# Performance work log

Hardware: AMD Instinct MI355X
Metric: run time of the kernel (lower is better)

## Reference

```python
import jax, jax.numpy as jnp
import numpy as np

B, D, K = 16384, 256, 1024

def setup_inputs() -> dict:
    key = jax.random.key(0)
    k1, k2 = jax.random.split(key)
    x = jax.random.normal(k1, (B, D), dtype=jnp.float32)
    centers = jax.random.uniform(k2, (K, D), dtype=jnp.float32)  # RandomUniform(0,1)
    betas = jnp.ones((K,), dtype=jnp.float32)
    return {"x": x, "centers": centers, "betas": betas}

def reference(x, centers, betas):
    x_sq = jnp.sum(x * x, axis=-1, keepdims=True)          # [B,1]
    c_sq = jnp.sum(centers * centers, axis=-1)             # [K]
    cross = jnp.einsum('bd,kd->bk', x, centers)            # [B,K]
    diffnorm = x_sq + c_sq[None, :] - 2.0 * cross          # [B,K]
    return jnp.exp(-betas[None, :] * diffnorm)             # [B,K]
```

## Files before the change

kernel.cpp:

```cpp
#include <hip/hip_runtime.h>
#include <stdint.h>

#define D_DIM 256
#define K_CTR 1024
#define B_ROWS 16384
#define BM 32

typedef float f32x4 __attribute__((ext_vector_type(4)));
typedef float f32x2 __attribute__((ext_vector_type(2)));
typedef long long i64x2 __attribute__((ext_vector_type(2)));

static __device__ __forceinline__ unsigned cvt4_fp8(const float4 v) {
    int r = __builtin_amdgcn_cvt_pk_fp8_f32(v.x, v.y, 0, false);
    r = __builtin_amdgcn_cvt_pk_fp8_f32(v.z, v.w, r, true);
    return (unsigned)r;
}

static __device__ __forceinline__ void barrier_lgkm() {
    asm volatile("s_waitcnt lgkmcnt(0)" ::: "memory");
    __builtin_amdgcn_s_barrier();
}

__global__ __launch_bounds__(256) void rbf_prep(const float* __restrict__ centers,
                                                unsigned char* __restrict__ cbf,
                                                float* __restrict__ csq) {
    const int w = threadIdx.x >> 6;
    const int l = threadIdx.x & 63;
    const int c0 = blockIdx.x * 4 + w;
    const float4 v = *reinterpret_cast<const float4*>(centers + c0 * D_DIM + l * 4);
    float s = v.x * v.x + v.y * v.y + v.z * v.z + v.w * v.w;
    const unsigned u = cvt4_fp8(v);
    const unsigned off = (unsigned)((c0 >> 4) * 4096 + (l >> 4) * 1024
                       + (((l >> 1) & 3) * 16 + (c0 & 15)) * 16
                       + ((l >> 3) & 1) * 8 + (l & 1) * 4);
    *reinterpret_cast<unsigned*>(cbf + off) = u;
    #pragma unroll
    for (int off2 = 1; off2 < 64; off2 <<= 1) s += __shfl_xor(s, off2);
    if (l == 0) csq[c0] = s;
}

__global__ __launch_bounds__(512, 4) void rbf_main(const float* __restrict__ x,
                                                   const unsigned char* __restrict__ cbf,
                                                   const float* __restrict__ csq,
                                                   const float* __restrict__ betas,
                                                   float* __restrict__ out) {
    __shared__ __align__(16) unsigned char As[BM * D_DIM];
    __shared__ __align__(16) float obuf[2][BM * 128];
    __shared__ float xs_lds[BM];

    const int tid = threadIdx.x;
    const int w = tid >> 6;
    const int l = tid & 63;
    const int strip = (blockIdx.x & 7) * 64 + (blockIdx.x >> 3);
    const int row0 = strip * BM;

    #pragma unroll
    for (int i = 0; i < 4; ++i) {
        const int r = i * 8 + w;
        const float4 v = *reinterpret_cast<const float4*>(x + (size_t)(row0 + r) * D_DIM + l * 4);
        float s = v.x * v.x + v.y * v.y + v.z * v.z + v.w * v.w;
        const unsigned u = cvt4_fp8(v);
        const unsigned pos = (unsigned)((l >> 4) * 64 + ((l >> 1) & 3) * 16
                           + ((l >> 3) & 1) * 8 + (l & 1) * 4);
        *reinterpret_cast<unsigned*>(As + r * 256 + (pos ^ ((unsigned)(r & 7) << 4))) = u;
        #pragma unroll
        for (int off = 1; off < 64; off <<= 1) s += __shfl_xor(s, off);
        if (l == 0) xs_lds[r] = s;
    }

    const int hk = l >> 4;
    const int lr = l & 15;
    const unsigned char* bwave = cbf + l * 16;

    i64x2 b0[4], b1[4];
    {
        const unsigned char* bbase = bwave + w * 4096;
        #pragma unroll
        for (int p = 0; p < 4; ++p)
            b0[p] = *reinterpret_cast<const i64x2*>(bbase + p * 1024);
    }
    barrier_lgkm();

    i64x2 a[2][4];
    #pragma unroll
    for (int m = 0; m < 2; ++m) {
        const int r = m * 16 + lr;
        #pragma unroll
        for (int p = 0; p < 4; ++p)
            a[m][p] = *reinterpret_cast<const i64x2*>(
                As + r * 256 + ((unsigned)(p * 64 + hk * 16) ^ ((unsigned)(lr & 7) << 4)));
    }
    const float xs0 = xs_lds[lr];
    const float xs1 = xs_lds[16 + lr];
    const float LOG2E = 1.4426950408889634f;

    #pragma unroll
    for (int ph = 0; ph < 8; ++ph) {
        const int colp = ph * 128;
        const i64x2 (&bc)[4] = (ph & 1) ? b1 : b0;
        i64x2 (&bn)[4] = (ph & 1) ? b0 : b1;

        if (ph < 7) {
            const unsigned char* bbase = bwave + ((ph + 1) * 8 + w) * 4096;
            #pragma unroll
            for (int p = 0; p < 4; ++p)
                bn[p] = *reinterpret_cast<const i64x2*>(bbase + p * 1024);
        }

        f32x4 acc[2] = {};
        #pragma unroll
        for (int p = 0; p < 4; ++p)
            #pragma unroll
            for (int m = 0; m < 2; ++m) {
                acc[m] = __builtin_amdgcn_mfma_f32_16x16x32_fp8_fp8(bc[p][0], a[m][p][0], acc[m], 0, 0, 0);
                acc[m] = __builtin_amdgcn_mfma_f32_16x16x32_fp8_fp8(bc[p][1], a[m][p][1], acc[m], 0, 0, 0);
            }

        float* ob = obuf[ph & 1];
        {
            const int cl = w * 16 + hk * 4;
            const f32x4 cs = *reinterpret_cast<const f32x4*>(csq + colp + cl);
            const f32x4 bt = *reinterpret_cast<const f32x4*>(betas + colp + cl);
            f32x4 btl2, coef2, base;
            #pragma unroll
            for (int j = 0; j < 4; ++j) {
                btl2[j] = bt[j] * LOG2E;
                coef2[j] = btl2[j] + btl2[j];
                base[j] = -btl2[j] * cs[j];
            }
            #pragma unroll
            for (int m = 0; m < 2; ++m) {
                const int r = m * 16 + lr;
                const float xsv = m ? xs1 : xs0;
                f32x4 rv;
                #pragma unroll
                for (int j = 0; j < 4; ++j) {
                    const float c0 = __builtin_fmaf(-btl2[j], xsv, base[j]);
                    rv[j] = __builtin_exp2f(__builtin_fmaf(coef2[j], acc[m][j], c0));
                }
                *reinterpret_cast<f32x4*>(reinterpret_cast<char*>(ob)
                    + r * 512 + ((unsigned)(cl * 4) ^ ((unsigned)(r & 7) << 4))) = rv;
            }
        }
        barrier_lgkm();

        #pragma unroll
        for (int i = 0; i < 4; ++i) {
            const int r = w * 4 + i;
            const f32x2 v = *reinterpret_cast<const f32x2*>(reinterpret_cast<const char*>(obuf[ph & 1])
                    + r * 512 + ((unsigned)(l * 8) ^ ((unsigned)(r & 7) << 4)));
            *reinterpret_cast<f32x2*>(out + (size_t)(row0 + r) * K_CTR + colp + l * 2) = v;
        }
    }
}

extern "C" void kernel_launch(void* const* d_in, const int* in_sizes, int n_in,
                              void* d_out, int out_size, void* d_ws, size_t ws_size,
                              hipStream_t stream) {
    const float* x       = (const float*)d_in[0];
    const float* centers = (const float*)d_in[1];
    const float* betas   = (const float*)d_in[2];
    float* out = (float*)d_out;

    unsigned char* cbf = (unsigned char*)d_ws;
    float* csq = (float*)((char*)d_ws + (size_t)K_CTR * D_DIM);

    rbf_prep<<<K_CTR / 4, 256, 0, stream>>>(centers, cbf, csq);
    rbf_main<<<B_ROWS / BM, 512, 0, stream>>>(x, cbf, csq, betas, out);
}
```

Measured before the change: 27.33 us.

## Restructure output staging into two full-row passes with 16-byte global stores

The main loop is reorganised so each 16-row half of the tile computes all 1024 columns before writing. Results are staged in a larger 64KB LDS buffer and flushed as whole rows with 128-bit global stores, replacing the per-128-column 64-bit stores. This cuts the barrier count from 8 to about 3 and makes the write stream more contiguous. The cost is doubled B-fragment reloads from global/L2 (16 phases instead of 8), half the MFMA work between loads, and more LDS per block, which may lower occupancy below the launch-bounds target.

```diff
diff --git a/kernel.cpp b/kernel.cpp
--- a/kernel.cpp
+++ b/kernel.cpp
@@ -7,7 +7,6 @@
 #define BM 32
 
 typedef float f32x4 __attribute__((ext_vector_type(4)));
-typedef float f32x2 __attribute__((ext_vector_type(2)));
 typedef long long i64x2 __attribute__((ext_vector_type(2)));
 
 static __device__ __forceinline__ unsigned cvt4_fp8(const float4 v) {
@@ -45,7 +44,7 @@
                                                    const float* __restrict__ betas,
                                                    float* __restrict__ out) {
     __shared__ __align__(16) unsigned char As[BM * D_DIM];
-    __shared__ __align__(16) float obuf[2][BM * 128];
+    __shared__ __align__(16) float obuf[16 * K_CTR];
     __shared__ float xs_lds[BM];
 
     const int tid = threadIdx.x;
@@ -83,74 +82,68 @@
 
     i64x2 a[2][4];
     #pragma unroll
-    for (int m = 0; m < 2; ++m) {
-        const int r = m * 16 + lr;
+    for (int s = 0; s < 2; ++s) {
+        const int r = s * 16 + lr;
         #pragma unroll
         for (int p = 0; p < 4; ++p)
-            a[m][p] = *reinterpret_cast<const i64x2*>(
+            a[s][p] = *reinterpret_cast<const i64x2*>(
                 As + r * 256 + ((unsigned)(p * 64 + hk * 16) ^ ((unsigned)(lr & 7) << 4)));
     }
-    const float xs0 = xs_lds[lr];
-    const float xs1 = xs_lds[16 + lr];
+    const float xsA[2] = { xs_lds[lr], xs_lds[16 + lr] };
     const float LOG2E = 1.4426950408889634f;
 
     #pragma unroll
-    for (int ph = 0; ph < 8; ++ph) {
-        const int colp = ph * 128;
-        const i64x2 (&bc)[4] = (ph & 1) ? b1 : b0;
-        i64x2 (&bn)[4] = (ph & 1) ? b0 : b1;
+    for (int s = 0; s < 2; ++s) {
+        #pragma unroll
+        for (int ph = 0; ph < 8; ++ph) {
+            const int t = s * 8 + ph;
+            const i64x2 (&bc)[4] = (t & 1) ? b1 : b0;
+            i64x2 (&bn)[4] = (t & 1) ? b0 : b1;
 
-        if (ph < 7) {
-            const unsigned char* bbase = bwave + ((ph + 1) * 8 + w) * 4096;
-            #pragma unroll
-            for (int p = 0; p < 4; ++p)
-                bn[p] = *reinterpret_cast<const i64x2*>(bbase + p * 1024);
-        }
-
-        f32x4 acc[2] = {};
-        #pragma unroll
-        for (int p = 0; p < 4; ++p)
-            #pragma unroll
-            for (int m = 0; m < 2; ++m) {
-                acc[m] = __builtin_amdgcn_mfma_f32_16x16x32_fp8_fp8(bc[p][0], a[m][p][0], acc[m], 0, 0, 0);
-                acc[m] = __builtin_amdgcn_mfma_f32_16x16x32_fp8_fp8(bc[p][1], a[m][p][1], acc[m], 0, 0, 0);
+            if (t < 15) {
+                const unsigned char* bbase = bwave + (((t + 1) & 7) * 8 + w) * 4096;
+                #pragma unroll
+                for (int p = 0; p < 4; ++p)
+                    bn[p] = *reinterpret_cast<const i64x2*>(bbase + p * 1024);
             }
 
-        float* ob = obuf[ph & 1];
-        {
-            const int cl = w * 16 + hk * 4;
-            const f32x4 cs = *reinterpret_cast<const f32x4*>(csq + colp + cl);
-            const f32x4 bt = *reinterpret_cast<const f32x4*>(betas + colp + cl);
-            f32x4 btl2, coef2, base;
+            f32x4 acc = {};
+            #pragma unroll
+            for (int p = 0; p < 4; ++p) {
+                acc = __builtin_amdgcn_mfma_f32_16x16x32_fp8_fp8(bc[p][0], a[s][p][0], acc, 0, 0, 0);
+                acc = __builtin_amdgcn_mfma_f32_16x16x32_fp8_fp8(bc[p][1], a[s][p][1], acc, 0, 0, 0);
+            }
+
+            const int cl = ph * 128 + w * 16 + hk * 4;
+            const f32x4 cs = *reinterpret_cast<const f32x4*>(csq + cl);
+            const f32x4 bt = *reinterpret_cast<const f32x4*>(betas + cl);
+            f32x4 rv;
             #pragma unroll
             for (int j = 0; j < 4; ++j) {
-                btl2[j] = bt[j] * LOG2E;
-                coef2[j] = btl2[j] + btl2[j];
-                base[j] = -btl2[j] * cs[j];
+                const float btl2 = bt[j] * LOG2E;
+                const float c0 = -btl2 * (xsA[s] + cs[j]);
+                rv[j] = __builtin_exp2f(__builtin_fmaf(btl2 + btl2, acc[j], c0));
             }
-            #pragma unroll
-            for (int m = 0; m < 2; ++m) {
-                const int r = m * 16 + lr;
-                const float xsv = m ? xs1 : xs0;
-                f32x4 rv;
-                #pragma unroll
-                for (int j = 0; j < 4; ++j) {
-                    const float c0 = __builtin_fmaf(-btl2[j], xsv, base[j]);
-                    rv[j] = __builtin_exp2f(__builtin_fmaf(coef2[j], acc[m][j], c0));
-                }
-                *reinterpret_cast<f32x4*>(reinterpret_cast<char*>(ob)
-                    + r * 512 + ((unsigned)(cl * 4) ^ ((unsigned)(r & 7) << 4))) = rv;
-            }
+            *reinterpret_cast<f32x4*>(reinterpret_cast<char*>(obuf)
+                + lr * 4096 + ((unsigned)(cl * 4) ^ ((unsigned)(lr & 7) << 4))) = rv;
         }
         barrier_lgkm();
 
         #pragma unroll
-        for (int i = 0; i < 4; ++i) {
-            const int r = w * 4 + i;
-            const f32x2 v = *reinterpret_cast<const f32x2*>(reinterpret_cast<const char*>(obuf[ph & 1])
-                    + r * 512 + ((unsigned)(l * 8) ^ ((unsigned)(r & 7) << 4)));
-            *reinterpret_cast<f32x2*>(out + (size_t)(row0 + r) * K_CTR + colp + l * 2) = v;
+        for (int j = 0; j < 2; ++j) {
+            const int r = w * 2 + j;
+            const unsigned sw = (unsigned)(r & 7) << 4;
+            f32x4 sv[4];
+            #pragma unroll
+            for (int c = 0; c < 4; ++c)
+                sv[c] = *reinterpret_cast<const f32x4*>(reinterpret_cast<const char*>(obuf)
+                        + r * 4096 + ((unsigned)(l * 16 + c * 1024) ^ sw));
+            float* orow = out + (size_t)(row0 + s * 16 + r) * K_CTR;
+            #pragma unroll
+            for (int c = 0; c < 4; ++c)
+                *reinterpret_cast<f32x4*>(orow + c * 256 + l * 4) = sv[c];
         }
+        if (s == 0) barrier_lgkm();
     }
 }
 
```

Result: slower. 32.32 us (+18.2%).

## Halve row tile to 16 with 4 waves each covering two column tiles

Applied to the files above, without the earlier changes.

Shrinks the row strip per block from 32 to 16 and the block from 8 to 4 waves. Each wave now computes two 16-column MFMA tiles against a single A fragment, instead of two row fragments against one column tile. The grid doubles to 1024 smaller blocks. The aim is better load balance and occupancy across CUs for this write-bound kernel. The cost is that the fp8 centers are re-read from L2 twice as often in total, and each wave holds more B registers.

```diff
diff --git a/kernel.cpp b/kernel.cpp
--- a/kernel.cpp
+++ b/kernel.cpp
@@ -4,7 +4,7 @@
 #define D_DIM 256
 #define K_CTR 1024
 #define B_ROWS 16384
-#define BM 32
+#define BM 16
 
 typedef float f32x4 __attribute__((ext_vector_type(4)));
 typedef float f32x2 __attribute__((ext_vector_type(2)));
@@ -39,7 +39,7 @@
     if (l == 0) csq[c0] = s;
 }
 
-__global__ __launch_bounds__(512, 4) void rbf_main(const float* __restrict__ x,
+__global__ __launch_bounds__(256, 4) void rbf_main(const float* __restrict__ x,
                                                    const unsigned char* __restrict__ cbf,
                                                    const float* __restrict__ csq,
                                                    const float* __restrict__ betas,
@@ -51,12 +51,12 @@
     const int tid = threadIdx.x;
     const int w = tid >> 6;
     const int l = tid & 63;
-    const int strip = (blockIdx.x & 7) * 64 + (blockIdx.x >> 3);
+    const int strip = (blockIdx.x & 7) * 128 + (blockIdx.x >> 3);
     const int row0 = strip * BM;
 
     #pragma unroll
     for (int i = 0; i < 4; ++i) {
-        const int r = i * 8 + w;
+        const int r = i * 4 + w;
         const float4 v = *reinterpret_cast<const float4*>(x + (size_t)(row0 + r) * D_DIM + l * 4);
         float s = v.x * v.x + v.y * v.y + v.z * v.z + v.w * v.w;
         const unsigned u = cvt4_fp8(v);
@@ -72,75 +72,64 @@
     const int lr = l & 15;
     const unsigned char* bwave = cbf + l * 16;
 
-    i64x2 b0[4], b1[4];
-    {
-        const unsigned char* bbase = bwave + w * 4096;
+    i64x2 b0[2][4], b1[2][4];
+    #pragma unroll
+    for (int e = 0; e < 2; ++e) {
+        const unsigned char* bbase = bwave + (w * 2 + e) * 4096;
         #pragma unroll
         for (int p = 0; p < 4; ++p)
-            b0[p] = *reinterpret_cast<const i64x2*>(bbase + p * 1024);
+            b0[e][p] = *reinterpret_cast<const i64x2*>(bbase + p * 1024);
     }
     barrier_lgkm();
 
-    i64x2 a[2][4];
+    i64x2 a[4];
     #pragma unroll
-    for (int m = 0; m < 2; ++m) {
-        const int r = m * 16 + lr;
-        #pragma unroll
-        for (int p = 0; p < 4; ++p)
-            a[m][p] = *reinterpret_cast<const i64x2*>(
-                As + r * 256 + ((unsigned)(p * 64 + hk * 16) ^ ((unsigned)(lr & 7) << 4)));
-    }
-    const float xs0 = xs_lds[lr];
-    const float xs1 = xs_lds[16 + lr];
+    for (int p = 0; p < 4; ++p)
+        a[p] = *reinterpret_cast<const i64x2*>(
+            As + lr * 256 + ((unsigned)(p * 64 + hk * 16) ^ ((unsigned)(lr & 7) << 4)));
+    const float xs = xs_lds[lr];
     const float LOG2E = 1.4426950408889634f;
 
     #pragma unroll
     for (int ph = 0; ph < 8; ++ph) {
         const int colp = ph * 128;
-        const i64x2 (&bc)[4] = (ph & 1) ? b1 : b0;
-        i64x2 (&bn)[4] = (ph & 1) ? b0 : b1;
+        const i64x2 (&bc)[2][4] = (ph & 1) ? b1 : b0;
+        i64x2 (&bn)[2][4] = (ph & 1) ? b0 : b1;
 
         if (ph < 7) {
-            const unsigned char* bbase = bwave + ((ph + 1) * 8 + w) * 4096;
             #pragma unroll
-            for (int p = 0; p < 4; ++p)
-                bn[p] = *reinterpret_cast<const i64x2*>(bbase + p * 1024);
+            for (int e = 0; e < 2; ++e) {
+                const unsigned char* bbase = bwave + ((ph + 1) * 8 + w * 2 + e) * 4096;
+                #pragma unroll
+                for (int p = 0; p < 4; ++p)
+                    bn[e][p] = *reinterpret_cast<const i64x2*>(bbase + p * 1024);
+            }
         }
 
         f32x4 acc[2] = {};
         #pragma unroll
         for (int p = 0; p < 4; ++p)
             #pragma unroll
-            for (int m = 0; m < 2; ++m) {
-                acc[m] = __builtin_amdgcn_mfma_f32_16x16x32_fp8_fp8(bc[p][0], a[m][p][0], acc[m], 0, 0, 0);
-                acc[m] = __builtin_amdgcn_mfma_f32_16x16x32_fp8_fp8(bc[p][1], a[m][p][1], acc[m], 0, 0, 0);
+            for (int e = 0; e < 2; ++e) {
+                acc[e] = __builtin_amdgcn_mfma_f32_16x16x32_fp8_fp8(bc[e][p][0], a[p][0], acc[e], 0, 0, 0);
+                acc[e] = __builtin_amdgcn_mfma_f32_16x16x32_fp8_fp8(bc[e][p][1], a[p][1], acc[e], 0, 0, 0);
             }
 
         float* ob = obuf[ph & 1];
-        {
-            const int cl = w * 16 + hk * 4;
+        #pragma unroll
+        for (int e = 0; e < 2; ++e) {
+            const int cl = (w * 2 + e) * 16 + hk * 4;
             const f32x4 cs = *reinterpret_cast<const f32x4*>(csq + colp + cl);
             const f32x4 bt = *reinterpret_cast<const f32x4*>(betas + colp + cl);
-            f32x4 btl2, coef2, base;
+            f32x4 rv;
             #pragma unroll
             for (int j = 0; j < 4; ++j) {
-                btl2[j] = bt[j] * LOG2E;
-                coef2[j] = btl2[j] + btl2[j];
-                base[j] = -btl2[j] * cs[j];
+                const float btl2 = bt[j] * LOG2E;
+                const float cc = -btl2 * (xs + cs[j]);
+                rv[j] = __builtin_exp2f(__builtin_fmaf(btl2 + btl2, acc[e][j], cc));
             }
-            #pragma unroll
-            for (int m = 0; m < 2; ++m) {
-                const int r = m * 16 + lr;
-                const float xsv = m ? xs1 : xs0;
-                f32x4 rv;
-                #pragma unroll
-                for (int j = 0; j < 4; ++j) {
-                    const float c0 = __builtin_fmaf(-btl2[j], xsv, base[j]);
-                    rv[j] = __builtin_exp2f(__builtin_fmaf(coef2[j], acc[m][j], c0));
-                }
-                *reinterpret_cast<f32x4*>(reinterpret_cast<char*>(ob)
-                    + r * 512 + ((unsigned)(cl * 4) ^ ((unsigned)(r & 7) << 4))) = rv;
-            }
+            *reinterpret_cast<f32x4*>(reinterpret_cast<char*>(ob)
+                + lr * 512 + ((unsigned)(cl * 4) ^ ((unsigned)(lr & 7) << 4))) = rv;
         }
         barrier_lgkm();
 
@@ -166,5 +155,5 @@
     float* csq = (float*)((char*)d_ws + (size_t)K_CTR * D_DIM);
 
     rbf_prep<<<K_CTR / 4, 256, 0, stream>>>(centers, cbf, csq);
-    rbf_main<<<B_ROWS / BM, 512, 0, stream>>>(x, cbf, csq, betas, out);
+    rbf_main<<<B_ROWS / BM, 256, 0, stream>>>(x, cbf, csq, betas, out);
 }
```

Measured after the change: 32.38 us. +18.5%, slower.

## Split each row strip across two blocks by column half with 256-thread blocks

Applied to the files above, without the earlier changes.

Each 32-row strip is now handled by two 256-thread blocks, each covering 512 of the 1024 centers, which doubles the grid to 1024 blocks and halves the LDS output buffer. The intent is better occupancy and load balance across CUs, at the cost of quantizing each x strip to fp8 twice. Output stores become scalar float per lane instead of float2. The epilogue coefficient math is also rearranged slightly.

```diff
diff --git a/kernel.cpp b/kernel.cpp
--- a/kernel.cpp
+++ b/kernel.cpp
@@ -7,7 +7,6 @@
 #define BM 32
 
 typedef float f32x4 __attribute__((ext_vector_type(4)));
-typedef float f32x2 __attribute__((ext_vector_type(2)));
 typedef long long i64x2 __attribute__((ext_vector_type(2)));
 
 static __device__ __forceinline__ unsigned cvt4_fp8(const float4 v) {
@@ -39,24 +38,26 @@
     if (l == 0) csq[c0] = s;
 }
 
-__global__ __launch_bounds__(512, 4) void rbf_main(const float* __restrict__ x,
+__global__ __launch_bounds__(256, 4) void rbf_main(const float* __restrict__ x,
                                                    const unsigned char* __restrict__ cbf,
                                                    const float* __restrict__ csq,
                                                    const float* __restrict__ betas,
                                                    float* __restrict__ out) {
     __shared__ __align__(16) unsigned char As[BM * D_DIM];
-    __shared__ __align__(16) float obuf[2][BM * 128];
+    __shared__ __align__(16) float obuf[2][BM * 64];
     __shared__ float xs_lds[BM];
 
     const int tid = threadIdx.x;
     const int w = tid >> 6;
     const int l = tid & 63;
-    const int strip = (blockIdx.x & 7) * 64 + (blockIdx.x >> 3);
+    const int swz = (blockIdx.x & 7) * 128 + (blockIdx.x >> 3);
+    const int strip = swz & 511;
+    const int cidx  = swz >> 9;
     const int row0 = strip * BM;
 
     #pragma unroll
-    for (int i = 0; i < 4; ++i) {
-        const int r = i * 8 + w;
+    for (int i = 0; i < 8; ++i) {
+        const int r = i * 4 + w;
         const float4 v = *reinterpret_cast<const float4*>(x + (size_t)(row0 + r) * D_DIM + l * 4);
         float s = v.x * v.x + v.y * v.y + v.z * v.z + v.w * v.w;
         const unsigned u = cvt4_fp8(v);
@@ -71,10 +72,11 @@
     const int hk = l >> 4;
     const int lr = l & 15;
     const unsigned char* bwave = cbf + l * 16;
+    const int cgbase = cidx * 32;
 
     i64x2 b0[4], b1[4];
     {
-        const unsigned char* bbase = bwave + w * 4096;
+        const unsigned char* bbase = bwave + (cgbase + w) * 4096;
         #pragma unroll
         for (int p = 0; p < 4; ++p)
             b0[p] = *reinterpret_cast<const i64x2*>(bbase + p * 1024);
@@ -96,12 +98,12 @@
 
     #pragma unroll
     for (int ph = 0; ph < 8; ++ph) {
-        const int colp = ph * 128;
+        const int colp = cidx * 512 + ph * 64;
         const i64x2 (&bc)[4] = (ph & 1) ? b1 : b0;
         i64x2 (&bn)[4] = (ph & 1) ? b0 : b1;
 
         if (ph < 7) {
-            const unsigned char* bbase = bwave + ((ph + 1) * 8 + w) * 4096;
+            const unsigned char* bbase = bwave + (cgbase + (ph + 1) * 4 + w) * 4096;
             #pragma unroll
             for (int p = 0; p < 4; ++p)
                 bn[p] = *reinterpret_cast<const i64x2*>(bbase + p * 1024);
@@ -121,13 +123,6 @@
             const int cl = w * 16 + hk * 4;
             const f32x4 cs = *reinterpret_cast<const f32x4*>(csq + colp + cl);
             const f32x4 bt = *reinterpret_cast<const f32x4*>(betas + colp + cl);
-            f32x4 btl2, coef2, base;
-            #pragma unroll
-            for (int j = 0; j < 4; ++j) {
-                btl2[j] = bt[j] * LOG2E;
-                coef2[j] = btl2[j] + btl2[j];
-                base[j] = -btl2[j] * cs[j];
-            }
             #pragma unroll
             for (int m = 0; m < 2; ++m) {
                 const int r = m * 16 + lr;
@@ -135,21 +130,22 @@
                 f32x4 rv;
                 #pragma unroll
                 for (int j = 0; j < 4; ++j) {
-                    const float c0 = __builtin_fmaf(-btl2[j], xsv, base[j]);
-                    rv[j] = __builtin_exp2f(__builtin_fmaf(coef2[j], acc[m][j], c0));
+                    const float btl2 = bt[j] * LOG2E;
+                    const float cc = -btl2 * (xsv + cs[j]);
+                    rv[j] = __builtin_exp2f(__builtin_fmaf(btl2 + btl2, acc[m][j], cc));
                 }
                 *reinterpret_cast<f32x4*>(reinterpret_cast<char*>(ob)
-                    + r * 512 + ((unsigned)(cl * 4) ^ ((unsigned)(r & 7) << 4))) = rv;
+                    + r * 256 + ((unsigned)(cl * 4) ^ ((unsigned)(r & 7) << 4))) = rv;
             }
         }
         barrier_lgkm();
 
         #pragma unroll
-        for (int i = 0; i < 4; ++i) {
-            const int r = w * 4 + i;
-            const f32x2 v = *reinterpret_cast<const f32x2*>(reinterpret_cast<const char*>(obuf[ph & 1])
-                    + r * 512 + ((unsigned)(l * 8) ^ ((unsigned)(r & 7) << 4)));
-            *reinterpret_cast<f32x2*>(out + (size_t)(row0 + r) * K_CTR + colp + l * 2) = v;
+        for (int i = 0; i < 8; ++i) {
+            const int r = w * 8 + i;
+            const float v = *reinterpret_cast<const float*>(reinterpret_cast<const char*>(obuf[ph & 1])
+                    + r * 256 + ((unsigned)(l * 4) ^ ((unsigned)(r & 7) << 4)));
+            out[(size_t)(row0 + r) * K_CTR + colp + l] = v;
         }
     }
 }
@@ -166,5 +162,5 @@
     float* csq = (float*)((char*)d_ws + (size_t)K_CTR * D_DIM);
 
     rbf_prep<<<K_CTR / 4, 256, 0, stream>>>(centers, cbf, csq);
-    rbf_main<<<B_ROWS / BM, 512, 0, stream>>>(x, cbf, csq, betas, out);
+    rbf_main<<<(B_ROWS / BM) * 2, 256, 0, stream>>>(x, cbf, csq, betas, out);
 }
```

Measured after the change: 29.60 us. 1.08x slower.
